# Optimization experiments

Hardware: AMD Instinct MI355X
Metric: run time of the kernel (lower is better)

## Reference

```python
import jax, jax.numpy as jnp
import numpy as np

KNN_K = 3  # module hard-codes top-3 farthest sememes (torch.sort descending)


def setup_inputs() -> dict:
    key = jax.random.key(0)
    k1, k2, k3 = jax.random.split(key, 3)
    V, H = 50257, 1024
    L, W, S = 256, 16, 32
    embedding = jax.random.normal(k1, (V, H), dtype=jnp.float32)
    word_ids = jax.random.randint(k2, (L, W), 0, V, dtype=jnp.int32)
    sememe_ids = jax.random.randint(k3, (L, W, S), 0, V, dtype=jnp.int32)
    return {"embedding": embedding, "word_ids": word_ids, "sememe_ids": sememe_ids}


def reference(embedding, word_ids, sememe_ids):
    # embedding: [V,H]; word_ids: [L,W]; sememe_ids: [L,W,S]
    w = embedding[word_ids]                  # [L,W,H]  word embeddings (s)
    sm = embedding[sememe_ids]               # [L,W,S,H] sememe embeddings
    # F.pairwise_distance(s, sememe_tensor, p=2): L2 per sememe
    dist = jnp.linalg.norm(sm - w[:, :, None, :], axis=-1)  # [L,W,S]
    # torch.sort(distance, descending=True)[1][:3] -> 3 farthest sememes
    _, idx = jax.lax.top_k(dist, KNN_K)                      # [L,W,K]
    sel = jnp.take_along_axis(sm, idx[..., None], axis=2)    # [L,W,K,H]
    # cat([knn_mean.unsqueeze(0), s], 0).mean(0) == (knn_mean + s) / 2
    per_word = 0.5 * (sel.mean(axis=2) + w)                  # [L,W,H]
    # stack(span).mean(0): mean over words in each label
    return per_word.mean(axis=1)                             # [L,H]
```

## Files before the change

kernel.cpp:

```cpp
#include <hip/hip_runtime.h>


#define HDIM 1024
#define SNUM 32
#define KNN  3

__global__ __launch_bounds__(256) void sememe_knn_kernel(
    const float* __restrict__ emb,
    const int*   __restrict__ word_ids,
    const int*   __restrict__ sem_ids,
    float*       __restrict__ out)
{
    const int b    = blockIdx.x;
    const int l    = b >> 4;
    const int t    = threadIdx.x;
    const int lane = t & 63;
    const int wave = t >> 6;

    __shared__ int   s_sid[SNUM];
    __shared__ float s_part[SNUM][4];
    __shared__ float s_dist[SNUM];
    __shared__ int   s_sel[KNN];

    if (t < SNUM) s_sid[t] = sem_ids[(size_t)b * SNUM + t];
    const int wid = word_ids[b];
    __syncthreads();

    const float4 wv = *reinterpret_cast<const float4*>(emb + (size_t)wid * HDIM + 4 * t);

    float dpart[SNUM];
    #pragma unroll
    for (int s = 0; s < SNUM; ++s) {
        const float4 sv = *reinterpret_cast<const float4*>(emb + (size_t)s_sid[s] * HDIM + 4 * t);
        const float dx = sv.x - wv.x;
        const float dy = sv.y - wv.y;
        const float dz = sv.z - wv.z;
        const float dw = sv.w - wv.w;
        dpart[s] = (dx * dx + dy * dy) + (dz * dz + dw * dw);
    }

    #pragma unroll
    for (int s = 0; s < SNUM; ++s) {
        float d = dpart[s];
        #pragma unroll
        for (int off = 32; off >= 1; off >>= 1)
            d += __shfl_xor(d, off, 64);
        if (lane == 0) s_part[s][wave] = d;
    }
    __syncthreads();
    if (t < SNUM)
        s_dist[t] = (s_part[t][0] + s_part[t][1]) + (s_part[t][2] + s_part[t][3]);
    __syncthreads();

    if (t == 0) {
        unsigned chosen = 0;
        for (int k = 0; k < KNN; ++k) {
            float best = -1.0f;
            int   bi   = 0;
            for (int s = 0; s < SNUM; ++s) {
                if (chosen & (1u << s)) continue;
                if (s_dist[s] > best) { best = s_dist[s]; bi = s; }
            }
            chosen |= (1u << bi);
            s_sel[k] = bi;
        }
    }
    __syncthreads();

    const float4 e0 = *reinterpret_cast<const float4*>(emb + (size_t)s_sid[s_sel[0]] * HDIM + 4 * t);
    const float4 e1 = *reinterpret_cast<const float4*>(emb + (size_t)s_sid[s_sel[1]] * HDIM + 4 * t);
    const float4 e2 = *reinterpret_cast<const float4*>(emb + (size_t)s_sid[s_sel[2]] * HDIM + 4 * t);

    const float third = 1.0f / 3.0f;
    const float scale = 0.5f / 16.0f;

    const float ox = ((e0.x + e1.x + e2.x) * third + wv.x) * scale;
    const float oy = ((e0.y + e1.y + e2.y) * third + wv.y) * scale;
    const float oz = ((e0.z + e1.z + e2.z) * third + wv.z) * scale;
    const float ow = ((e0.w + e1.w + e2.w) * third + wv.w) * scale;

    float* op = out + (size_t)l * HDIM + 4 * t;
    atomicAdd(op + 0, ox);
    atomicAdd(op + 1, oy);
    atomicAdd(op + 2, oz);
    atomicAdd(op + 3, ow);
}

extern "C" void kernel_launch(void* const* d_in, const int* in_sizes, int n_in,
                              void* d_out, int out_size, void* d_ws, size_t ws_size,
                              hipStream_t stream) {
    const float* emb  = (const float*)d_in[0];
    const int*   wids = (const int*)d_in[1];
    const int*   sids = (const int*)d_in[2];
    float*       out  = (float*)d_out;

    const int n_words = in_sizes[1];

    hipMemsetAsync(d_out, 0, (size_t)out_size * sizeof(float), stream);
    sememe_knn_kernel<<<dim3(n_words), dim3(256), 0, stream>>>(emb, wids, sids, out);
}
```

Before: 112.7 us.

## Split fused KNN kernel into distance, select, and reduce kernels

Replaces the single per-word kernel with three launches. The first computes each word-sememe distance with one wave per pair, the second does top-3 selection with one thread per word, and the third gathers the selected rows and reduces over the 16 words per label without atomics. This removes the memset, the float atomics and the serial single-thread top-k inside each block, and gives more parallelism to the distance stage. In exchange it adds two kernel launches, workspace traffic and a second gather of the embedding rows, and the select kernel runs only 4096 threads.

```diff
diff --git a/kernel.cpp b/kernel.cpp
--- a/kernel.cpp
+++ b/kernel.cpp
@@ -3,87 +3,115 @@
 
 #define HDIM 1024
 #define SNUM 32
+#define WNUM 16
 #define KNN  3
 
-__global__ __launch_bounds__(256) void sememe_knn_kernel(
+__global__ __launch_bounds__(256) void knn_dist_kernel(
     const float* __restrict__ emb,
     const int*   __restrict__ word_ids,
     const int*   __restrict__ sem_ids,
-    float*       __restrict__ out)
+    float*       __restrict__ dist,
+    int nj)
 {
-    const int b    = blockIdx.x;
-    const int l    = b >> 4;
-    const int t    = threadIdx.x;
-    const int lane = t & 63;
-    const int wave = t >> 6;
+    const int wave = threadIdx.x >> 6;
+    const int lane = threadIdx.x & 63;
+    const int j    = blockIdx.x * 4 + wave;
+    if (j >= nj) return;
+    const int b    = j >> 5;
 
-    __shared__ int   s_sid[SNUM];
-    __shared__ float s_part[SNUM][4];
-    __shared__ float s_dist[SNUM];
-    __shared__ int   s_sel[KNN];
+    const int wid = word_ids[b];
+    const int sid = sem_ids[j];
 
-    if (t < SNUM) s_sid[t] = sem_ids[(size_t)b * SNUM + t];
-    const int wid = word_ids[b];
-    __syncthreads();
+    const float* wrow = emb + (size_t)wid * HDIM + 4 * lane;
+    const float* srow = emb + (size_t)sid * HDIM + 4 * lane;
 
-    const float4 wv = *reinterpret_cast<const float4*>(emb + (size_t)wid * HDIM + 4 * t);
+    const float4 w0 = *(const float4*)(wrow + 0);
+    const float4 w1 = *(const float4*)(wrow + 256);
+    const float4 w2 = *(const float4*)(wrow + 512);
+    const float4 w3 = *(const float4*)(wrow + 768);
+    const float4 s0 = *(const float4*)(srow + 0);
+    const float4 s1 = *(const float4*)(srow + 256);
+    const float4 s2 = *(const float4*)(srow + 512);
+    const float4 s3 = *(const float4*)(srow + 768);
 
-    float dpart[SNUM];
-    #pragma unroll
-    for (int s = 0; s < SNUM; ++s) {
-        const float4 sv = *reinterpret_cast<const float4*>(emb + (size_t)s_sid[s] * HDIM + 4 * t);
-        const float dx = sv.x - wv.x;
-        const float dy = sv.y - wv.y;
-        const float dz = sv.z - wv.z;
-        const float dw = sv.w - wv.w;
-        dpart[s] = (dx * dx + dy * dy) + (dz * dz + dw * dw);
+    float d = 0.0f;
+    {
+        float dx = s0.x - w0.x, dy = s0.y - w0.y, dz = s0.z - w0.z, dw = s0.w - w0.w;
+        d += dx * dx + dy * dy + dz * dz + dw * dw;
+    }
+    {
+        float dx = s1.x - w1.x, dy = s1.y - w1.y, dz = s1.z - w1.z, dw = s1.w - w1.w;
+        d += dx * dx + dy * dy + dz * dz + dw * dw;
+    }
+    {
+        float dx = s2.x - w2.x, dy = s2.y - w2.y, dz = s2.z - w2.z, dw = s2.w - w2.w;
+        d += dx * dx + dy * dy + dz * dz + dw * dw;
+    }
+    {
+        float dx = s3.x - w3.x, dy = s3.y - w3.y, dz = s3.z - w3.z, dw = s3.w - w3.w;
+        d += dx * dx + dy * dy + dz * dz + dw * dw;
     }
 
     #pragma unroll
-    for (int s = 0; s < SNUM; ++s) {
-        float d = dpart[s];
+    for (int off = 32; off >= 1; off >>= 1)
+        d += __shfl_xor(d, off, 64);
+
+    if (lane == 0) dist[j] = d;
+}
+
+__global__ __launch_bounds__(256) void knn_select_kernel(
+    const float* __restrict__ dist,
+    const int*   __restrict__ word_ids,
+    const int*   __restrict__ sem_ids,
+    int*         __restrict__ sel,
+    int nb)
+{
+    const int b = blockIdx.x * 256 + threadIdx.x;
+    if (b >= nb) return;
+
+    float dl[SNUM];
+    #pragma unroll
+    for (int s = 0; s < SNUM; ++s) dl[s] = dist[b * SNUM + s];
+
+    unsigned chosen = 0;
+    #pragma unroll
+    for (int k = 0; k < KNN; ++k) {
+        float best = -1.0f;
+        int   bi   = 0;
         #pragma unroll
-        for (int off = 32; off >= 1; off >>= 1)
-            d += __shfl_xor(d, off, 64);
-        if (lane == 0) s_part[s][wave] = d;
+        for (int s = 0; s < SNUM; ++s) {
+            if (!((chosen >> s) & 1u) && dl[s] > best) { best = dl[s]; bi = s; }
+        }
+        chosen |= (1u << bi);
+        sel[b * 4 + k] = sem_ids[b * SNUM + bi];
     }
-    __syncthreads();
-    if (t < SNUM)
-        s_dist[t] = (s_part[t][0] + s_part[t][1]) + (s_part[t][2] + s_part[t][3]);
+    sel[b * 4 + 3] = word_ids[b];
+}
+
+__global__ __launch_bounds__(256) void knn_out_kernel(
+    const float* __restrict__ emb,
+    const int*   __restrict__ sel,
+    float*       __restrict__ out)
+{
+    const int l = blockIdx.x >> 2;
+    const int q = blockIdx.x & 3;
+    const int h = q * 256 + threadIdx.x;
+
+    __shared__ int s_ids[WNUM * 4];
+    if (threadIdx.x < WNUM * 4) s_ids[threadIdx.x] = sel[l * WNUM * 4 + threadIdx.x];
     __syncthreads();
 
-    if (t == 0) {
-        unsigned chosen = 0;
-        for (int k = 0; k < KNN; ++k) {
-            float best = -1.0f;
-            int   bi   = 0;
-            for (int s = 0; s < SNUM; ++s) {
-                if (chosen & (1u << s)) continue;
-                if (s_dist[s] > best) { best = s_dist[s]; bi = s; }
-            }
-            chosen |= (1u << bi);
-            s_sel[k] = bi;
-        }
+    const float third = 1.0f / 3.0f;
+    float acc = 0.0f;
+    #pragma unroll
+    for (int w = 0; w < WNUM; ++w) {
+        const float e0 = emb[(size_t)s_ids[w * 4 + 0] * HDIM + h];
+        const float e1 = emb[(size_t)s_ids[w * 4 + 1] * HDIM + h];
+        const float e2 = emb[(size_t)s_ids[w * 4 + 2] * HDIM + h];
+        const float ew = emb[(size_t)s_ids[w * 4 + 3] * HDIM + h];
+        acc += (e0 + e1 + e2) * third + ew;
     }
-    __syncthreads();
-
-    const float4 e0 = *reinterpret_cast<const float4*>(emb + (size_t)s_sid[s_sel[0]] * HDIM + 4 * t);
-    const float4 e1 = *reinterpret_cast<const float4*>(emb + (size_t)s_sid[s_sel[1]] * HDIM + 4 * t);
-    const float4 e2 = *reinterpret_cast<const float4*>(emb + (size_t)s_sid[s_sel[2]] * HDIM + 4 * t);
-
-    const float third = 1.0f / 3.0f;
-    const float scale = 0.5f / 16.0f;
-
-    const float ox = ((e0.x + e1.x + e2.x) * third + wv.x) * scale;
-    const float oy = ((e0.y + e1.y + e2.y) * third + wv.y) * scale;
-    const float oz = ((e0.z + e1.z + e2.z) * third + wv.z) * scale;
-    const float ow = ((e0.w + e1.w + e2.w) * third + wv.w) * scale;
-
-    float* op = out + (size_t)l * HDIM + 4 * t;
-    atomicAdd(op + 0, ox);
-    atomicAdd(op + 1, oy);
-    atomicAdd(op + 2, oz);
-    atomicAdd(op + 3, ow);
+    out[(size_t)l * HDIM + h] = acc * (0.5f / 16.0f);
 }
 
 extern "C" void kernel_launch(void* const* d_in, const int* in_sizes, int n_in,
@@ -94,8 +122,14 @@
     const int*   sids = (const int*)d_in[2];
     float*       out  = (float*)d_out;
 
-    const int n_words = in_sizes[1];
+    const int nb = in_sizes[1];
+    const int nj = in_sizes[2];
+    const int L  = out_size / HDIM;
 
-    hipMemsetAsync(d_out, 0, (size_t)out_size * sizeof(float), stream);
-    sememe_knn_kernel<<<dim3(n_words), dim3(256), 0, stream>>>(emb, wids, sids, out);
+    float* dist = (float*)d_ws;
+    int*   sel  = (int*)((char*)d_ws + (size_t)nj * 4);
+
+    knn_dist_kernel<<<dim3((nj + 3) / 4), dim3(256), 0, stream>>>(emb, wids, sids, dist, nj);
+    knn_select_kernel<<<dim3((nb + 255) / 256), dim3(256), 0, stream>>>(dist, wids, sids, sel, nb);
+    knn_out_kernel<<<dim3(L * 4), dim3(256), 0, stream>>>(emb, sel, out);
 }
```

Result: faster. 107.6 us (-4.6%).
